# Kernel tuning notes

Measured on AMD Instinct MI355X. Metric: run time of the kernel, lower is better.

Reference implementation:

```python
import jax, jax.numpy as jnp
import numpy as np

N = 50000      # nodes
E = 800000     # edges (avg degree 16)
F_IN = 32      # raw node feature dim
H = 96         # hidden_channels == encoder.output_dim (skip_connection=True)
EDGE_DIM = 16
L = 3          # num_layers
B = 50         # graphs in batch
MSG_IN = 2 * H + 1 + EDGE_DIM   # [h_i, h_j, ||dpos||^2, edge_attr]
NODE_IN = 2 * H                 # [h_i, aggregated message]


def setup_inputs() -> dict:
    key = jax.random.key(0)
    ks = jax.random.split(key, 14)

    def w(k, shape):
        fan_in = shape[-2]
        return jax.random.normal(k, shape, jnp.float32) * (1.0 / np.sqrt(fan_in))

    return {
        "x": jax.random.normal(ks[0], (N, F_IN), jnp.float32),
        "pos": jax.random.normal(ks[1], (N, 3), jnp.float32),
        "edge_index": jax.random.randint(ks[2], (2, E), 0, N),
        "edge_attr": jax.random.normal(ks[3], (E, EDGE_DIM), jnp.float32),
        "batch_indices": jnp.sort(jax.random.randint(ks[4], (N,), 0, B)),
        # encoder (modeled as a linear projection to H)
        "We": w(ks[5], (F_IN, H)), "be": jnp.zeros((H,), jnp.float32),
        # per-layer EGNN edge MLP: Linear(MSG_IN,H)-SiLU-Linear(H,H)-SiLU
        "eW1": w(ks[6], (L, MSG_IN, H)), "eb1": jnp.zeros((L, H), jnp.float32),
        "eW2": w(ks[7], (L, H, H)), "eb2": jnp.zeros((L, H), jnp.float32),
        # per-layer EGNN node MLP: Linear(NODE_IN,H)-SiLU-Linear(H,H)
        "nW1": w(ks[8], (L, NODE_IN, H)), "nb1": jnp.zeros((L, H), jnp.float32),
        "nW2": w(ks[9], (L, H, H)), "nb2": jnp.zeros((L, H), jnp.float32),
        "Wl": w(ks[10], (H, 1)), "bl": jnp.zeros((1,), jnp.float32),
    }


def reference(x, pos, edge_index, edge_attr, batch_indices,
              We, be, eW1, eb1, eW2, eb2, nW1, nb1, nW2, nb2, Wl, bl):
    silu = jax.nn.silu
    src, dst = edge_index[0], edge_index[1]

    # encoder: project raw features to hidden dim
    h = x @ We + be                                    # [N, H]

    # squared pairwise distances along edges (pos fixed, update_pos=False)
    rel = pos[src] - pos[dst]                          # [E, 3]
    d2 = jnp.sum(rel * rel, axis=-1, keepdims=True)    # [E, 1]

    for l in range(L):
        feat = jnp.concatenate([h[src], h[dst], d2, edge_attr], axis=-1)  # [E, MSG_IN]
        m = silu(silu(feat @ eW1[l] + eb1[l]) @ eW2[l] + eb2[l])          # [E, H]
        agg = jax.ops.segment_sum(m, dst, num_segments=N)                 # [N, H]
        upd = silu(jnp.concatenate([h, agg], axis=-1) @ nW1[l] + nb1[l]) @ nW2[l] + nb2[l]
        h = h + upd  # skip_connection=True

    # global_mean_pool over graphs
    counts = jax.ops.segment_sum(jnp.ones((N, 1), h.dtype), batch_indices, num_segments=B)
    pooled = jax.ops.segment_sum(h, batch_indices, num_segments=B) / jnp.maximum(counts, 1.0)

    return pooled @ Wl + bl                            # [B, 1]
```

## Files before the change

kernel.cpp:

```cpp
#include <hip/hip_runtime.h>

#define Nn 50000
#define Ee 800000
#define FIN 32
#define EDIM 16
#define Bb 50
#define SPX 6250

typedef _Float16 half8 __attribute__((ext_vector_type(8)));
typedef float floatx4 __attribute__((ext_vector_type(4)));

#define OFF_WeT 0
#define WT_LAYER(l) (3072 + (l) * 58368)
#define OFF_W1AB 0
#define OFF_W1C  18432
#define OFF_W2   21504
#define OFF_NW1  30720
#define OFF_NW2  49152
#define WT_TOTAL 178176

__device__ __forceinline__ float silu_f(float x) {
    return __fdividef(x, 1.0f + __expf(-x));
}

__device__ __forceinline__ int lower_bound_i(const int* a, int n, int v) {
    int lo = 0, hi = n;
    while (lo < hi) { int m = (lo + hi) >> 1; if (a[m] < v) lo = m + 1; else hi = m; }
    return lo;
}

__device__ __forceinline__ half8 ldg_h8(const _Float16* p) {
    return *(const half8*)p;
}

__device__ __forceinline__ half8 h8_zero() {
    half8 z;
    #pragma unroll
    for (int j = 0; j < 8; j++) z[j] = (_Float16)0.f;
    return z;
}

__global__ void k_prepw(const float* __restrict__ We, const float* __restrict__ eW1,
                        const float* __restrict__ eW2, const float* __restrict__ nW1,
                        const float* __restrict__ nW2, _Float16* __restrict__ wT) {
    int idx = blockIdx.x * 256 + threadIdx.x;
    if (idx >= WT_TOTAL) return;
    float v;
    if (idx < 3072) {
        int n = idx >> 5, k = idx & 31;
        v = We[k * 96 + n];
    } else {
        int j = idx - 3072;
        int l = j / 58368, r = j % 58368;
        const float* eW1l = eW1 + l * 209 * 96;
        if (r < 18432) {
            int n = r / 96, k = r % 96;
            v = (n < 96) ? eW1l[k * 96 + n] : eW1l[(96 + k) * 96 + (n - 96)];
        } else if (r < 21504) {
            int r2 = r - 18432;
            int n = r2 >> 5, k = r2 & 31;
            v = (k < 16) ? eW1l[(193 + k) * 96 + n]
              : (k == 16) ? eW1l[192 * 96 + n] : 0.f;
        } else if (r < 30720) {
            int r2 = r - 21504;
            int n = r2 / 96, k = r2 % 96;
            v = eW2[l * 9216 + k * 96 + n];
        } else if (r < 49152) {
            int r2 = r - 30720;
            int n = r2 / 192, k = r2 % 192;
            v = nW1[l * 18432 + k * 96 + n];
        } else {
            int r2 = r - 49152;
            int n = r2 / 96, k = r2 % 96;
            v = nW2[l * 9216 + k * 96 + n];
        }
    }
    wT[idx] = (_Float16)v;
}

__global__ void k_prep(const int* __restrict__ ei, const float* __restrict__ pos,
                       float* __restrict__ d2, int* __restrict__ counts) {
    int e = blockIdx.x * 256 + threadIdx.x;
    if (e >= Ee) return;
    int s = ei[e], d = ei[Ee + e];
    float dx = pos[s * 3 + 0] - pos[d * 3 + 0];
    float dy = pos[s * 3 + 1] - pos[d * 3 + 1];
    float dz = pos[s * 3 + 2] - pos[d * 3 + 2];
    d2[e] = dx * dx + dy * dy + dz * dz;
    atomicAdd(&counts[d], 1);
}

__global__ void k_scanA(const int* __restrict__ counts, int* __restrict__ rowstart,
                        int* __restrict__ bsums) {
    __shared__ int s[256];
    int b = blockIdx.x, t = threadIdx.x, i = b * 256 + t;
    int v = (i < Nn) ? counts[i] : 0;
    s[t] = v;
    __syncthreads();
    for (int off = 1; off < 256; off <<= 1) {
        int add = (t >= off) ? s[t - off] : 0;
        __syncthreads();
        s[t] += add;
        __syncthreads();
    }
    if (i < Nn) rowstart[i + 1] = s[t];
    if (t == 255) bsums[b] = s[255];
}

__global__ void k_scanB(int* __restrict__ bsums, int nb) {
    __shared__ int s[256];
    int t = threadIdx.x;
    int v = (t < nb) ? bsums[t] : 0;
    s[t] = v;
    __syncthreads();
    for (int off = 1; off < 256; off <<= 1) {
        int add = (t >= off) ? s[t - off] : 0;
        __syncthreads();
        s[t] += add;
        __syncthreads();
    }
    if (t < nb) bsums[t] = s[t] - v;
}

__global__ void k_scanC(int* __restrict__ rowstart, const int* __restrict__ bsums) {
    int b = blockIdx.x, t = threadIdx.x, i = b * 256 + t;
    if (i < Nn) rowstart[i + 1] += bsums[b];
    if (i == 0 && b == 0) rowstart[0] = 0;
}

__global__ void k_fill(const int* __restrict__ ei, const float* __restrict__ ea,
                       const float* __restrict__ d2, const int* __restrict__ rowstart,
                       int* __restrict__ cur, int* __restrict__ srcs_p,
                       int* __restrict__ dsts_p, _Float16* __restrict__ eap16,
                       _Float16* __restrict__ d2h) {
    int e = blockIdx.x * 256 + threadIdx.x;
    if (e >= Ee) return;
    int s = ei[e], d = ei[Ee + e];
    int slot = rowstart[d] + atomicAdd(&cur[d], 1);
    srcs_p[slot] = s;
    dsts_p[slot] = d;
    const float4* ea4 = (const float4*)ea;
    float4 q0 = ea4[e * 4 + 0], q1 = ea4[e * 4 + 1];
    float4 q2 = ea4[e * 4 + 2], q3 = ea4[e * 4 + 3];
    half8 c0, c1;
    c0[0]=(_Float16)q0.x; c0[1]=(_Float16)q0.y; c0[2]=(_Float16)q0.z; c0[3]=(_Float16)q0.w;
    c0[4]=(_Float16)q1.x; c0[5]=(_Float16)q1.y; c0[6]=(_Float16)q1.z; c0[7]=(_Float16)q1.w;
    c1[0]=(_Float16)q2.x; c1[1]=(_Float16)q2.y; c1[2]=(_Float16)q2.z; c1[3]=(_Float16)q2.w;
    c1[4]=(_Float16)q3.x; c1[5]=(_Float16)q3.y; c1[6]=(_Float16)q3.z; c1[7]=(_Float16)q3.w;
    half8* dst8 = (half8*)(eap16 + (size_t)slot * 16);
    dst8[0] = c0; dst8[1] = c1;
    d2h[slot] = (_Float16)d2[e];
}

__global__ __launch_bounds__(256, 4)
void k_encab(const float* __restrict__ x, const _Float16* __restrict__ WeT,
             const float* __restrict__ be, const _Float16* __restrict__ W1abT,
             _Float16* __restrict__ h16, _Float16* __restrict__ A16,
             _Float16* __restrict__ B16, float* __restrict__ agg) {
    __shared__ _Float16 x16[64][40];
    __shared__ _Float16 hs[64][104];
    int t = threadIdx.x;
    int n0 = blockIdx.x * 64;
    for (int i = t; i < 64 * 32; i += 256) {
        int nl = i >> 5, k = i & 31;
        int n = n0 + nl;
        x16[nl][k] = (_Float16)((n < Nn) ? x[n * FIN + k] : 0.f);
    }
    __syncthreads();
    int lane = t & 63, quad = lane >> 4, lm = lane & 15, w = t >> 6;
    half8 af = *(const half8*)&x16[w * 16 + lm][quad * 8];
    for (int nt = 0; nt < 6; nt++) {
        int col = nt * 16 + lm;
        float b = be[col];
        floatx4 acc = {b, b, b, b};
        half8 bf = ldg_h8(WeT + col * 32 + quad * 8);
        acc = __builtin_amdgcn_mfma_f32_16x16x32_f16(af, bf, acc, 0, 0, 0);
        #pragma unroll
        for (int r = 0; r < 4; r++)
            hs[w * 16 + quad * 4 + r][col] = (_Float16)acc[r];
    }
    __syncthreads();
    #pragma unroll
    for (int i = 0; i < 3; i++) {
        int ci = t + 256 * i;
        int el = ci / 12, c0 = (ci % 12) * 8;
        int n = n0 + el;
        if (n < Nn) *(half8*)(h16 + n * 96 + c0) = *(half8*)&hs[el][c0];
    }
    for (int i = t; i < 64 * 24; i += 256) {
        int el = i / 24, c = (i % 24) * 4;
        int n = n0 + el;
        if (n < Nn) *(float4*)(agg + n * 96 + c) = make_float4(0.f, 0.f, 0.f, 0.f);
    }
    half8 af3[3];
    #pragma unroll
    for (int kt = 0; kt < 3; kt++)
        af3[kt] = *(const half8*)&hs[w * 16 + lm][kt * 32 + quad * 8];
    for (int nt = 0; nt < 12; nt++) {
        int col = nt * 16 + lm;
        floatx4 acc = {0.f, 0.f, 0.f, 0.f};
        #pragma unroll
        for (int kt = 0; kt < 3; kt++) {
            half8 bf = ldg_h8(W1abT + col * 96 + kt * 32 + quad * 8);
            acc = __builtin_amdgcn_mfma_f32_16x16x32_f16(af3[kt], bf, acc, 0, 0, 0);
        }
        #pragma unroll
        for (int r = 0; r < 4; r++) {
            int n = n0 + w * 16 + quad * 4 + r;
            if (n < Nn) {
                if (col < 96) A16[n * 96 + col] = (_Float16)acc[r];
                else          B16[n * 96 + col - 96] = (_Float16)acc[r];
            }
        }
    }
}

__global__ __launch_bounds__(256, 4)
void k_edge(const _Float16* __restrict__ A16, const _Float16* __restrict__ B16,
            const _Float16* __restrict__ eap16, const _Float16* __restrict__ d2h,
            const int* __restrict__ srcs_p, const int* __restrict__ dsts_p,
            const _Float16* __restrict__ W1cT, const float* __restrict__ eb1l,
            const _Float16* __restrict__ W2T, const float* __restrict__ eb2l,
            float* __restrict__ agg) {
    __shared__ _Float16 u16[64][104];
    __shared__ _Float16 W2f[18 * 64 * 8];
    __shared__ _Float16 W1f[6 * 64 * 8];
    __shared__ int ss_s[4][16], ds_s[4][16];

    int t = threadIdx.x;
    int lane = t & 63, quad = lane >> 4, lm = lane & 15, w = t >> 6;

    for (int f = w; f < 18; f += 4) {
        int nt = f / 3, kt = f % 3;
        half8 v = ldg_h8(W2T + (nt * 16 + lm) * 96 + kt * 32 + quad * 8);
        *(half8*)&W2f[(f * 64 + lane) * 8] = v;
    }
    for (int f = w; f < 6; f += 4) {
        half8 v = ldg_h8(W1cT + (f * 16 + lm) * 32 + quad * 8);
        *(half8*)&W1f[(f * 64 + lane) * 8] = v;
    }
    float eb1v[6], eb2v[6];
    #pragma unroll
    for (int nt = 0; nt < 6; nt++) {
        eb1v[nt] = eb1l[nt * 16 + lm];
        eb2v[nt] = eb2l[nt * 16 + lm];
    }
    __syncthreads();

    int xcd = blockIdx.x & 7, ib = blockIdx.x >> 3;
    int slot = ib * 4 + w;
    for (int s = slot; s < SPX; s += 512) {
        int e0 = (xcd * SPX + s) * 16;
        half8 af1;
        if (quad == 0)      af1 = ldg_h8(eap16 + (size_t)(e0 + lm) * 16);
        else if (quad == 1) af1 = ldg_h8(eap16 + (size_t)(e0 + lm) * 16 + 8);
        else { af1 = h8_zero(); if (quad == 2) af1[0] = d2h[e0 + lm]; }
        if (lane < 16) {
            ss_s[w][lane] = srcs_p[e0 + lane];
            ds_s[w][lane] = dsts_p[e0 + lane];
        }
        #pragma unroll
        for (int nt = 0; nt < 6; nt++) {
            floatx4 acc = {eb1v[nt], eb1v[nt], eb1v[nt], eb1v[nt]};
            half8 bf = *(const half8*)&W1f[(nt * 64 + lane) * 8];
            acc = __builtin_amdgcn_mfma_f32_16x16x32_f16(af1, bf, acc, 0, 0, 0);
            #pragma unroll
            for (int r = 0; r < 4; r++)
                u16[w * 16 + quad * 4 + r][nt * 16 + lm] = (_Float16)acc[r];
        }
        #pragma unroll
        for (int i = 0; i < 3; i++) {
            int ci = lane + 64 * i;
            int el = ci / 12, c0 = (ci % 12) * 8;
            half8 av = ldg_h8(A16 + ss_s[w][el] * 96 + c0);
            half8 bv = ldg_h8(B16 + ds_s[w][el] * 96 + c0);
            half8 pv = *(half8*)&u16[w * 16 + el][c0];
            half8 sum = pv + av + bv;
            half8 res;
            #pragma unroll
            for (int j = 0; j < 8; j++)
                res[j] = (_Float16)silu_f((float)sum[j]);
            *(half8*)&u16[w * 16 + el][c0] = res;
        }
        half8 af2[3];
        #pragma unroll
        for (int kt = 0; kt < 3; kt++)
            af2[kt] = *(const half8*)&u16[w * 16 + lm][kt * 32 + quad * 8];
        #pragma unroll
        for (int nt = 0; nt < 6; nt++) {
            floatx4 acc = {eb2v[nt], eb2v[nt], eb2v[nt], eb2v[nt]};
            #pragma unroll
            for (int kt = 0; kt < 3; kt++) {
                half8 bf = *(const half8*)&W2f[((nt * 3 + kt) * 64 + lane) * 8];
                acc = __builtin_amdgcn_mfma_f32_16x16x32_f16(af2[kt], bf, acc, 0, 0, 0);
            }
            #pragma unroll
            for (int r = 0; r < 4; r++)
                u16[w * 16 + quad * 4 + r][nt * 16 + lm] = (_Float16)silu_f(acc[r]);
        }
        #pragma unroll
        for (int p = 0; p < 2; p++) {
            int c = lane + p * 64;
            if (c < 96) {
                float run = 0.f;
                int cd = ds_s[w][0];
                #pragma unroll
                for (int e = 0; e < 16; e++) {
                    int dn = ds_s[w][e];
                    if (dn != cd) { atomicAdd(&agg[cd * 96 + c], run); run = 0.f; cd = dn; }
                    run += (float)u16[w * 16 + e][c];
                }
                atomicAdd(&agg[cd * 96 + c], run);
            }
        }
    }
}

__global__ __launch_bounds__(256, 4)
void k_nodeab(_Float16* __restrict__ h16, float* __restrict__ agg,
              const _Float16* __restrict__ nW1T, const float* __restrict__ nb1l,
              const _Float16* __restrict__ nW2T, const float* __restrict__ nb2l,
              const _Float16* __restrict__ W1abT, _Float16* __restrict__ A16,
              _Float16* __restrict__ B16, int do_ab) {
    __shared__ _Float16 in16[64][200];
    __shared__ _Float16 t116[64][104];
    int t = threadIdx.x, n0 = blockIdx.x * 64;
    #pragma unroll
    for (int i = 0; i < 3; i++) {
        int ci = t + 256 * i;
        int el = ci / 12, c0 = (ci % 12) * 8;
        int n = n0 + el;
        half8 hv = h8_zero();
        half8 av = h8_zero();
        if (n < Nn) {
            hv = ldg_h8(h16 + n * 96 + c0);
            float4 a = *(const float4*)(agg + n * 96 + c0);
            float4 b = *(const float4*)(agg + n * 96 + c0 + 4);
            av[0]=(_Float16)a.x; av[1]=(_Float16)a.y; av[2]=(_Float16)a.z; av[3]=(_Float16)a.w;
            av[4]=(_Float16)b.x; av[5]=(_Float16)b.y; av[6]=(_Float16)b.z; av[7]=(_Float16)b.w;
        }
        *(half8*)&in16[el][c0] = hv;
        *(half8*)&in16[el][96 + c0] = av;
    }
    __syncthreads();
    int lane = t & 63, quad = lane >> 4, lm = lane & 15, w = t >> 6;
    half8 af[6];
    #pragma unroll
    for (int kt = 0; kt < 6; kt++)
        af[kt] = *(const half8*)&in16[w * 16 + lm][kt * 32 + quad * 8];
    for (int nt = 0; nt < 6; nt++) {
        int col = nt * 16 + lm;
        float b = nb1l[col];
        floatx4 acc = {b, b, b, b};
        #pragma unroll
        for (int kt = 0; kt < 6; kt++) {
            half8 bf = ldg_h8(nW1T + col * 192 + kt * 32 + quad * 8);
            acc = __builtin_amdgcn_mfma_f32_16x16x32_f16(af[kt], bf, acc, 0, 0, 0);
        }
        #pragma unroll
        for (int r = 0; r < 4; r++)
            t116[w * 16 + quad * 4 + r][col] = (_Float16)silu_f(acc[r]);
    }
    half8 af2[3];
    #pragma unroll
    for (int kt = 0; kt < 3; kt++)
        af2[kt] = *(const half8*)&t116[w * 16 + lm][kt * 32 + quad * 8];
    for (int nt = 0; nt < 6; nt++) {
        int col = nt * 16 + lm;
        float b = nb2l[col];
        floatx4 acc = {b, b, b, b};
        #pragma unroll
        for (int kt = 0; kt < 3; kt++) {
            half8 bf = ldg_h8(nW2T + col * 96 + kt * 32 + quad * 8);
            acc = __builtin_amdgcn_mfma_f32_16x16x32_f16(af2[kt], bf, acc, 0, 0, 0);
        }
        #pragma unroll
        for (int r = 0; r < 4; r++) {
            int row = w * 16 + quad * 4 + r;
            float hnew = (float)in16[row][col] + acc[r];
            in16[row][col] = (_Float16)hnew;
        }
    }
    __syncthreads();
    #pragma unroll
    for (int i = 0; i < 3; i++) {
        int ci = t + 256 * i;
        int el = ci / 12, c0 = (ci % 12) * 8;
        int n = n0 + el;
        if (n < Nn) *(half8*)(h16 + n * 96 + c0) = *(half8*)&in16[el][c0];
    }
    if (!do_ab) return;
    half8 af3[3];
    #pragma unroll
    for (int kt = 0; kt < 3; kt++)
        af3[kt] = *(const half8*)&in16[w * 16 + lm][kt * 32 + quad * 8];
    for (int nt = 0; nt < 12; nt++) {
        int col = nt * 16 + lm;
        floatx4 acc = {0.f, 0.f, 0.f, 0.f};
        #pragma unroll
        for (int kt = 0; kt < 3; kt++) {
            half8 bf = ldg_h8(W1abT + col * 96 + kt * 32 + quad * 8);
            acc = __builtin_amdgcn_mfma_f32_16x16x32_f16(af3[kt], bf, acc, 0, 0, 0);
        }
        #pragma unroll
        for (int r = 0; r < 4; r++) {
            int n = n0 + w * 16 + quad * 4 + r;
            if (n < Nn) {
                if (col < 96) A16[n * 96 + col] = (_Float16)acc[r];
                else          B16[n * 96 + col - 96] = (_Float16)acc[r];
            }
        }
    }
    for (int i = t; i < 64 * 24; i += 256) {
        int el = i / 24, c = (i % 24) * 4;
        int n = n0 + el;
        if (n < Nn) *(float4*)(agg + n * 96 + c) = make_float4(0.f, 0.f, 0.f, 0.f);
    }
}

__global__ void k_pool_partial(const _Float16* __restrict__ h16, const int* __restrict__ batch,
                               float* __restrict__ pooled) {
    int g = blockIdx.x >> 2, q = blockIdx.x & 3;
    int start = lower_bound_i(batch, Nn, g);
    int end   = lower_bound_i(batch, Nn, g + 1);
    int len = end - start;
    int chunk = (len + 3) >> 2;
    int s = start + q * chunk;
    int e = min(s + chunk, end);
    int t = threadIdx.x;
    int j = t % 96, r = t / 96;
    float sum = 0.f;
    for (int n = s + r; n < e; n += 2) sum += (float)h16[n * 96 + j];
    atomicAdd(&pooled[g * 96 + j], sum);
}

__global__ void k_final(const float* __restrict__ pooled, const int* __restrict__ batch,
                        const float* __restrict__ Wl, const float* __restrict__ bl,
                        float* __restrict__ out) {
    int g = blockIdx.x, lane = threadIdx.x;
    int start = lower_bound_i(batch, Nn, g);
    int end   = lower_bound_i(batch, Nn, g + 1);
    int cnt = end - start; if (cnt < 1) cnt = 1;
    float v = 0.f;
    for (int j = lane; j < 96; j += 64) v += pooled[g * 96 + j] * Wl[j];
    #pragma unroll
    for (int off = 32; off > 0; off >>= 1) v += __shfl_down(v, off);
    if (lane == 0) out[g] = v / (float)cnt + bl[0];
}

extern "C" void kernel_launch(void* const* d_in, const int* in_sizes, int n_in,
                              void* d_out, int out_size, void* d_ws, size_t ws_size,
                              hipStream_t stream) {
    const float* x     = (const float*)d_in[0];
    const float* pos   = (const float*)d_in[1];
    const int*   ei    = (const int*)d_in[2];
    const float* ea    = (const float*)d_in[3];
    const int*   batch = (const int*)d_in[4];
    const float* We    = (const float*)d_in[5];
    const float* be    = (const float*)d_in[6];
    const float* eW1   = (const float*)d_in[7];
    const float* eb1   = (const float*)d_in[8];
    const float* eW2   = (const float*)d_in[9];
    const float* eb2   = (const float*)d_in[10];
    const float* nW1   = (const float*)d_in[11];
    const float* nb1   = (const float*)d_in[12];
    const float* nW2   = (const float*)d_in[13];
    const float* nb2   = (const float*)d_in[14];
    const float* Wl    = (const float*)d_in[15];
    const float* bl    = (const float*)d_in[16];
    float* out = (float*)d_out;

    float* ws = (float*)d_ws;
    _Float16* h16    = (_Float16*)(ws);
    _Float16* A16    = (_Float16*)(ws + 2400000);
    _Float16* B16    = (_Float16*)(ws + 4800000);
    float*    agg    = ws + 7200000;
    float*    d2     = ws + 12000000;
    float*    pooled = ws + 12800000;
    int*      counts   = (int*)(ws + 12804800);
    int*      cur      = (int*)(ws + 12854800);
    int*      rowstart = (int*)(ws + 12904800);
    int*      bsums    = (int*)(ws + 12954816);
    int*      srcs_p   = (int*)(ws + 12955072);
    int*      dsts_p   = (int*)(ws + 13755072);
    _Float16* eap16    = (_Float16*)(ws + 14555072);
    _Float16* d2h      = (_Float16*)(ws + 20955072);
    _Float16* wT       = (_Float16*)(ws + 21355072);

    hipMemsetAsync(counts, 0, 2 * 50000 * sizeof(int), stream);
    hipMemsetAsync(pooled, 0, Bb * 96 * sizeof(float), stream);

    k_prepw<<<dim3(696), dim3(256), 0, stream>>>(We, eW1, eW2, nW1, nW2, wT);
    k_prep<<<dim3(3125), dim3(256), 0, stream>>>(ei, pos, d2, counts);
    k_scanA<<<dim3(196), dim3(256), 0, stream>>>(counts, rowstart, bsums);
    k_scanB<<<dim3(1), dim3(256), 0, stream>>>(bsums, 196);
    k_scanC<<<dim3(196), dim3(256), 0, stream>>>(rowstart, bsums);
    k_fill<<<dim3(3125), dim3(256), 0, stream>>>(ei, ea, d2, rowstart, cur,
                                                 srcs_p, dsts_p, eap16, d2h);
    k_encab<<<dim3(782), dim3(256), 0, stream>>>(x, wT + OFF_WeT, be,
        wT + WT_LAYER(0) + OFF_W1AB, h16, A16, B16, agg);

    for (int l = 0; l < 3; l++) {
        const _Float16* wl = wT + WT_LAYER(l);
        k_edge<<<dim3(1024), dim3(256), 0, stream>>>(A16, B16, eap16, d2h,
            srcs_p, dsts_p, wl + OFF_W1C, eb1 + l * 96, wl + OFF_W2, eb2 + l * 96, agg);
        const _Float16* wnext = wT + WT_LAYER(l < 2 ? l + 1 : 0);
        k_nodeab<<<dim3(782), dim3(256), 0, stream>>>(h16, agg,
            wl + OFF_NW1, nb1 + l * 96, wl + OFF_NW2, nb2 + l * 96,
            wnext + OFF_W1AB, A16, B16, (l < 2) ? 1 : 0);
    }
    k_pool_partial<<<dim3(200), dim3(192), 0, stream>>>(h16, batch, pooled);
    k_final<<<dim3(50), dim3(64), 0, stream>>>(pooled, batch, Wl, bl, out);
}
```

Before: 743.5 us.

## Compute edge distances in fill kernel, unroll MFMA loops, pair-wise segment atomics

Edge squared distances are now computed directly in the CSR fill kernel rather than in a separate prep pass that wrote an fp32 d2 buffer, so k_prep only counts degrees. Several MFMA output-tile loops get explicit unroll pragmas. The edge kernel's segmented reduction now has 48 lanes each handle two adjacent channels instead of looping over two lane passes. These changes aim to cut global memory traffic and loop overhead, at the cost of higher register pressure from unrolling.

```diff
diff --git a/kernel.cpp b/kernel.cpp
--- a/kernel.cpp
+++ b/kernel.cpp
@@ -78,16 +78,10 @@
     wT[idx] = (_Float16)v;
 }
 
-__global__ void k_prep(const int* __restrict__ ei, const float* __restrict__ pos,
-                       float* __restrict__ d2, int* __restrict__ counts) {
+__global__ void k_prep(const int* __restrict__ ei, int* __restrict__ counts) {
     int e = blockIdx.x * 256 + threadIdx.x;
     if (e >= Ee) return;
-    int s = ei[e], d = ei[Ee + e];
-    float dx = pos[s * 3 + 0] - pos[d * 3 + 0];
-    float dy = pos[s * 3 + 1] - pos[d * 3 + 1];
-    float dz = pos[s * 3 + 2] - pos[d * 3 + 2];
-    d2[e] = dx * dx + dy * dy + dz * dz;
-    atomicAdd(&counts[d], 1);
+    atomicAdd(&counts[ei[Ee + e]], 1);
 }
 
 __global__ void k_scanA(const int* __restrict__ counts, int* __restrict__ rowstart,
@@ -129,7 +123,7 @@
 }
 
 __global__ void k_fill(const int* __restrict__ ei, const float* __restrict__ ea,
-                       const float* __restrict__ d2, const int* __restrict__ rowstart,
+                       const float* __restrict__ pos, const int* __restrict__ rowstart,
                        int* __restrict__ cur, int* __restrict__ srcs_p,
                        int* __restrict__ dsts_p, _Float16* __restrict__ eap16,
                        _Float16* __restrict__ d2h) {
@@ -139,6 +133,10 @@
     int slot = rowstart[d] + atomicAdd(&cur[d], 1);
     srcs_p[slot] = s;
     dsts_p[slot] = d;
+    float dx = pos[s * 3 + 0] - pos[d * 3 + 0];
+    float dy = pos[s * 3 + 1] - pos[d * 3 + 1];
+    float dz = pos[s * 3 + 2] - pos[d * 3 + 2];
+    float dv = dx * dx + dy * dy + dz * dz;
     const float4* ea4 = (const float4*)ea;
     float4 q0 = ea4[e * 4 + 0], q1 = ea4[e * 4 + 1];
     float4 q2 = ea4[e * 4 + 2], q3 = ea4[e * 4 + 3];
@@ -149,7 +147,7 @@
     c1[4]=(_Float16)q3.x; c1[5]=(_Float16)q3.y; c1[6]=(_Float16)q3.z; c1[7]=(_Float16)q3.w;
     half8* dst8 = (half8*)(eap16 + (size_t)slot * 16);
     dst8[0] = c0; dst8[1] = c1;
-    d2h[slot] = (_Float16)d2[e];
+    d2h[slot] = (_Float16)dv;
 }
 
 __global__ __launch_bounds__(256, 4)
@@ -169,6 +167,7 @@
     __syncthreads();
     int lane = t & 63, quad = lane >> 4, lm = lane & 15, w = t >> 6;
     half8 af = *(const half8*)&x16[w * 16 + lm][quad * 8];
+    #pragma unroll
     for (int nt = 0; nt < 6; nt++) {
         int col = nt * 16 + lm;
         float b = be[col];
@@ -196,6 +195,7 @@
     #pragma unroll
     for (int kt = 0; kt < 3; kt++)
         af3[kt] = *(const half8*)&hs[w * 16 + lm][kt * 32 + quad * 8];
+    #pragma unroll
     for (int nt = 0; nt < 12; nt++) {
         int col = nt * 16 + lm;
         floatx4 acc = {0.f, 0.f, 0.f, 0.f};
@@ -298,20 +298,25 @@
             for (int r = 0; r < 4; r++)
                 u16[w * 16 + quad * 4 + r][nt * 16 + lm] = (_Float16)silu_f(acc[r]);
         }
-        #pragma unroll
-        for (int p = 0; p < 2; p++) {
-            int c = lane + p * 64;
-            if (c < 96) {
-                float run = 0.f;
-                int cd = ds_s[w][0];
-                #pragma unroll
-                for (int e = 0; e < 16; e++) {
-                    int dn = ds_s[w][e];
-                    if (dn != cd) { atomicAdd(&agg[cd * 96 + c], run); run = 0.f; cd = dn; }
-                    run += (float)u16[w * 16 + e][c];
+        if (lane < 48) {
+            int c = lane * 2;
+            float run0 = 0.f, run1 = 0.f;
+            int cd = ds_s[w][0];
+            #pragma unroll
+            for (int e = 0; e < 16; e++) {
+                int dn = ds_s[w][e];
+                if (dn != cd) {
+                    atomicAdd(&agg[cd * 96 + c], run0);
+                    atomicAdd(&agg[cd * 96 + c + 1], run1);
+                    run0 = 0.f; run1 = 0.f; cd = dn;
                 }
-                atomicAdd(&agg[cd * 96 + c], run);
+                _Float16 v0 = u16[w * 16 + e][c];
+                _Float16 v1 = u16[w * 16 + e][c + 1];
+                run0 += (float)v0;
+                run1 += (float)v1;
             }
+            atomicAdd(&agg[cd * 96 + c], run0);
+            atomicAdd(&agg[cd * 96 + c + 1], run1);
         }
     }
 }
@@ -348,6 +353,7 @@
     #pragma unroll
     for (int kt = 0; kt < 6; kt++)
         af[kt] = *(const half8*)&in16[w * 16 + lm][kt * 32 + quad * 8];
+    #pragma unroll
     for (int nt = 0; nt < 6; nt++) {
         int col = nt * 16 + lm;
         float b = nb1l[col];
@@ -365,6 +371,7 @@
     #pragma unroll
     for (int kt = 0; kt < 3; kt++)
         af2[kt] = *(const half8*)&t116[w * 16 + lm][kt * 32 + quad * 8];
+    #pragma unroll
     for (int nt = 0; nt < 6; nt++) {
         int col = nt * 16 + lm;
         float b = nb2l[col];
@@ -394,6 +401,7 @@
     #pragma unroll
     for (int kt = 0; kt < 3; kt++)
         af3[kt] = *(const half8*)&in16[w * 16 + lm][kt * 32 + quad * 8];
+    #pragma unroll
     for (int nt = 0; nt < 12; nt++) {
         int col = nt * 16 + lm;
         floatx4 acc = {0.f, 0.f, 0.f, 0.f};
@@ -475,27 +483,26 @@
     _Float16* A16    = (_Float16*)(ws + 2400000);
     _Float16* B16    = (_Float16*)(ws + 4800000);
     float*    agg    = ws + 7200000;
-    float*    d2     = ws + 12000000;
-    float*    pooled = ws + 12800000;
-    int*      counts   = (int*)(ws + 12804800);
-    int*      cur      = (int*)(ws + 12854800);
-    int*      rowstart = (int*)(ws + 12904800);
-    int*      bsums    = (int*)(ws + 12954816);
-    int*      srcs_p   = (int*)(ws + 12955072);
-    int*      dsts_p   = (int*)(ws + 13755072);
-    _Float16* eap16    = (_Float16*)(ws + 14555072);
-    _Float16* d2h      = (_Float16*)(ws + 20955072);
-    _Float16* wT       = (_Float16*)(ws + 21355072);
+    float*    pooled = ws + 12000000;
+    int*      counts   = (int*)(ws + 12004800);
+    int*      cur      = (int*)(ws + 12054800);
+    int*      rowstart = (int*)(ws + 12104800);
+    int*      bsums    = (int*)(ws + 12154816);
+    int*      srcs_p   = (int*)(ws + 12155072);
+    int*      dsts_p   = (int*)(ws + 12955072);
+    _Float16* eap16    = (_Float16*)(ws + 13755072);
+    _Float16* d2h      = (_Float16*)(ws + 20155072);
+    _Float16* wT       = (_Float16*)(ws + 20555072);
 
     hipMemsetAsync(counts, 0, 2 * 50000 * sizeof(int), stream);
     hipMemsetAsync(pooled, 0, Bb * 96 * sizeof(float), stream);
 
     k_prepw<<<dim3(696), dim3(256), 0, stream>>>(We, eW1, eW2, nW1, nW2, wT);
-    k_prep<<<dim3(3125), dim3(256), 0, stream>>>(ei, pos, d2, counts);
+    k_prep<<<dim3(3125), dim3(256), 0, stream>>>(ei, counts);
     k_scanA<<<dim3(196), dim3(256), 0, stream>>>(counts, rowstart, bsums);
     k_scanB<<<dim3(1), dim3(256), 0, stream>>>(bsums, 196);
     k_scanC<<<dim3(196), dim3(256), 0, stream>>>(rowstart, bsums);
-    k_fill<<<dim3(3125), dim3(256), 0, stream>>>(ei, ea, d2, rowstart, cur,
+    k_fill<<<dim3(3125), dim3(256), 0, stream>>>(ei, ea, pos, rowstart, cur,
                                                  srcs_p, dsts_p, eap16, d2h);
     k_encab<<<dim3(782), dim3(256), 0, stream>>>(x, wT + OFF_WeT, be,
         wT + WT_LAYER(0) + OFF_W1AB, h16, A16, B16, agg);
```

After: 761.4 us. 1.02x slower.
